# Optimization experiments

Hardware: AMD Instinct MI355X
Metric: run time of the kernel (lower is better)

## Reference

```python
import jax, jax.numpy as jnp
import numpy as np

EPS = 1e-6   # param.eps
DT = 1e-2    # param.dt
DX = 1.0     # param.dx
DY = 1.0     # param.dy
N_PARAM = 1.0  # param.N


def _lap(c, dx=1.0, dy=1.0):
    # 5-point periodic Laplacian stencil on the last two dims
    return ((jnp.roll(c, 1, -1) + jnp.roll(c, -1, -1) - 2.0 * c) / (dx * dx)
            + (jnp.roll(c, 1, -2) + jnp.roll(c, -1, -2) - 2.0 * c) / (dy * dy))


def _log_with_mask(m, eps=EPS):
    # masked positions get constant eps -> zero gradient there, like torch masked_fill
    return jnp.log(jnp.where(m < eps, eps, m))


def setup_inputs() -> dict:
    key = jax.random.key(0)
    ks = jax.random.split(key, 12)
    B, H, W = 8, 1024, 1024
    inp = {
        "cv": jax.random.uniform(ks[0], (B, H, W), dtype=jnp.float32),
        "ci": jax.random.uniform(ks[1], (B, H, W), dtype=jnp.float32),
        "eta": jax.random.uniform(ks[2], (B, H, W), dtype=jnp.float32),
    }
    names = ["energy_v0", "energy_i0", "kBT0", "kappa_v0", "kappa_i0",
             "kappa_eta0", "diff_v0", "diff_i0", "L0"]
    for i, n in enumerate(names):
        inp[n] = jax.random.uniform(ks[3 + i], (1,), dtype=jnp.float32)
    return inp


def reference(cv, ci, eta, energy_v0, energy_i0, kBT0, kappa_v0, kappa_i0,
              kappa_eta0, diff_v0, diff_i0, L0):
    energy_v = jnp.abs(energy_v0) + 0.001
    energy_i = jnp.abs(energy_i0) + 0.001
    kBT = jnp.abs(kBT0) + 0.001
    kappa_v = jnp.abs(kappa_v0) + 0.001
    kappa_i = jnp.abs(kappa_i0) + 0.001
    kappa_eta = jnp.abs(kappa_eta0) + 0.001
    diff_v = jnp.abs(diff_v0) + 0.001
    diff_i = jnp.abs(diff_i0) + 0.001
    L = jnp.abs(L0) + 0.001

    lap_cv = _lap(cv, DX, DY)
    lap_ci = _lap(ci, DX, DY)
    lap_eta = _lap(eta, DX, DY)

    h = (eta - 1.0) ** 2
    j = eta ** 2
    cs = 1.0 - cv - ci
    log_cv = _log_with_mask(cv)
    log_ci = _log_with_mask(ci)
    log_cs = _log_with_mask(cs)

    fs = energy_v * cv + energy_i * ci + kBT * (cv * log_cv + ci * log_ci + cs * log_cs)
    dfs_dcv = energy_v + kBT * (log_cv - log_cs)
    dfs_dci = energy_i + kBT * (log_ci - log_cs)

    fv = (cv - 1.0) ** 2 + ci ** 2
    dfv_dcv = 2.0 * (cv - 1.0)
    dfv_dci = 2.0 * ci

    dF_dcv = h * dfs_dcv + j * dfv_dcv - kappa_v * lap_cv
    dF_dci = h * dfs_dci + j * dfv_dci - kappa_i * lap_ci
    dF_deta = N_PARAM * (fs * 2.0 * (eta - 1.0) + fv * 2.0 * eta - kappa_eta * lap_eta)

    mv = diff_v * cv / kBT
    mi = diff_i * ci / kBT

    cv_new = jnp.clip(cv + DT * (mv * _lap(dF_dcv)), 0.0, 1.0)
    ci_new = jnp.clip(ci + DT * (mi * _lap(dF_dci)), 0.0, 1.0)
    eta_new = jnp.clip(eta + DT * (-L * dF_deta), 0.0, 1.0)
    return cv_new, ci_new, eta_new
```

## Files before the change

kernel.cpp:

```cpp
#include <hip/hip_runtime.h>

#define WMASK 1023
#define LOG2W 10
#define HW (1024 * 1024)

#define EPS 1e-6f
#define DT 1e-2f

#define TX 64
#define TY 16
#define EX (TX + 2)
#define EY (TY + 2)

__device__ __forceinline__ float scal(const float* __restrict__ p) {
    return fabsf(p[0]) + 0.001f;
}
__device__ __forceinline__ float logm(float m) {
    return logf(m < EPS ? EPS : m);
}
__device__ __forceinline__ float clip01(float v) {
    return fminf(fmaxf(v, 0.0f), 1.0f);
}

__global__ __launch_bounds__(256) void irr_fused(
    const float* __restrict__ cv,
    const float* __restrict__ ci,
    const float* __restrict__ eta,
    const float* __restrict__ p_ev,
    const float* __restrict__ p_ei,
    const float* __restrict__ p_kbt,
    const float* __restrict__ p_kv,
    const float* __restrict__ p_ki,
    const float* __restrict__ p_ke,
    const float* __restrict__ p_dv,
    const float* __restrict__ p_di,
    const float* __restrict__ p_L,
    float* __restrict__ cv_new,
    float* __restrict__ ci_new,
    float* __restrict__ eta_new)
{
    __shared__ float sdv[EY][EX];
    __shared__ float sdi[EY][EX];

    const int tid = threadIdx.y * 64 + threadIdx.x;
    const int x0 = blockIdx.x * TX;
    const int y0 = blockIdx.y * TY;
    const int bbase = blockIdx.z * HW;

    const float energy_v = scal(p_ev);
    const float energy_i = scal(p_ei);
    const float kBT      = scal(p_kbt);
    const float kappa_v  = scal(p_kv);
    const float kappa_i  = scal(p_ki);
    const float kappa_e  = scal(p_ke);
    const float diff_v   = scal(p_dv);
    const float diff_i   = scal(p_di);
    const float L        = scal(p_L);

    for (int t = tid; t < EX * EY; t += 256) {
        const int ex = t % EX;
        const int ey = t / EX;
        const int gx = (x0 + ex - 1) & WMASK;
        const int gy = (y0 + ey - 1) & WMASK;
        const int row  = bbase + (gy << LOG2W);
        const int rowm = bbase + (((gy + WMASK) & WMASK) << LOG2W);
        const int rowp = bbase + (((gy + 1) & WMASK) << LOG2W);
        const int xm = (gx + WMASK) & WMASK;
        const int xp = (gx + 1) & WMASK;

        const float c0 = cv[row + gx];
        const float lap_cv = cv[row + xm] + cv[row + xp]
                           + cv[rowm + gx] + cv[rowp + gx] - 4.0f * c0;
        const float i0 = ci[row + gx];
        const float lap_ci = ci[row + xm] + ci[row + xp]
                           + ci[rowm + gx] + ci[rowp + gx] - 4.0f * i0;
        const float e0 = eta[row + gx];
        const float lap_eta = eta[row + xm] + eta[row + xp]
                            + eta[rowm + gx] + eta[rowp + gx] - 4.0f * e0;

        const float h  = (e0 - 1.0f) * (e0 - 1.0f);
        const float jj = e0 * e0;
        const float cs = 1.0f - c0 - i0;
        const float lcv = logm(c0);
        const float lci = logm(i0);
        const float lcs = logm(cs);

        const float fs = energy_v * c0 + energy_i * i0
                       + kBT * (c0 * lcv + i0 * lci + cs * lcs);
        const float dfs_dcv = energy_v + kBT * (lcv - lcs);
        const float dfs_dci = energy_i + kBT * (lci - lcs);

        const float fv = (c0 - 1.0f) * (c0 - 1.0f) + i0 * i0;
        const float dfv_dcv = 2.0f * (c0 - 1.0f);
        const float dfv_dci = 2.0f * i0;

        sdv[ey][ex] = h * dfs_dcv + jj * dfv_dcv - kappa_v * lap_cv;
        sdi[ey][ex] = h * dfs_dci + jj * dfv_dci - kappa_i * lap_ci;

        if (ex >= 1 && ex <= TX && ey >= 1 && ey <= TY) {
            const float dF_deta = fs * 2.0f * (e0 - 1.0f) + fv * 2.0f * e0
                                - kappa_e * lap_eta;
            eta_new[row + gx] = clip01(e0 + DT * (-L * dF_deta));
        }
    }

    __syncthreads();

    const int tx = threadIdx.x;
    for (int ty = threadIdx.y; ty < TY; ty += 4) {
        const int ex = tx + 1;
        const int ey = ty + 1;

        const float v0 = sdv[ey][ex];
        const float lap_v = sdv[ey][ex - 1] + sdv[ey][ex + 1]
                          + sdv[ey - 1][ex] + sdv[ey + 1][ex] - 4.0f * v0;
        const float w0 = sdi[ey][ex];
        const float lap_i = sdi[ey][ex - 1] + sdi[ey][ex + 1]
                          + sdi[ey - 1][ex] + sdi[ey + 1][ex] - 4.0f * w0;

        const int gidx = bbase + ((y0 + ty) << LOG2W) + (x0 + tx);
        const float c0 = cv[gidx];
        const float i0 = ci[gidx];

        const float mv = diff_v * c0 / kBT;
        const float mi = diff_i * i0 / kBT;

        cv_new[gidx] = clip01(c0 + DT * (mv * lap_v));
        ci_new[gidx] = clip01(i0 + DT * (mi * lap_i));
    }
}

extern "C" void kernel_launch(void* const* d_in, const int* in_sizes, int n_in,
                              void* d_out, int out_size, void* d_ws, size_t ws_size,
                              hipStream_t stream) {
    const float* cv  = (const float*)d_in[0];
    const float* ci  = (const float*)d_in[1];
    const float* eta = (const float*)d_in[2];
    const float* p_ev  = (const float*)d_in[3];
    const float* p_ei  = (const float*)d_in[4];
    const float* p_kbt = (const float*)d_in[5];
    const float* p_kv  = (const float*)d_in[6];
    const float* p_ki  = (const float*)d_in[7];
    const float* p_ke  = (const float*)d_in[8];
    const float* p_dv  = (const float*)d_in[9];
    const float* p_di  = (const float*)d_in[10];
    const float* p_L   = (const float*)d_in[11];

    const int N = in_sizes[0];

    float* out     = (float*)d_out;
    float* cv_new  = out;
    float* ci_new  = out + N;
    float* eta_new = out + 2 * N;

    const dim3 block(64, 4, 1);
    const dim3 grid(1024 / TX, 1024 / TY, N / HW);

    irr_fused<<<grid, block, 0, stream>>>(cv, ci, eta, p_ev, p_ei, p_kbt,
                                          p_kv, p_ki, p_ke, p_dv, p_di, p_L,
                                          cv_new, ci_new, eta_new);
}
```

Baseline: 232.3 us.

## Stage input tiles in shared memory with float4 loads and nontemporal stores

Each block now loads a 20x72 halo tile of cv, ci and eta into shared memory with vectorized float4 loads, then computes both stencil passes from LDS instead of issuing redundant scattered global reads. Also switches to fast __logf, precomputes diff/kBT, and writes outputs with nontemporal stores. The trade-offs are much larger shared memory use per block, which may lower occupancy, and slightly less accurate logarithms.

Result: faster. 208.3 us (-10.3%).

```diff
diff --git a/kernel.cpp b/kernel.cpp
--- a/kernel.cpp
+++ b/kernel.cpp
@@ -9,14 +9,16 @@
 
 #define TX 64
 #define TY 16
-#define EX (TX + 2)
-#define EY (TY + 2)
+#define RX 72
+#define RY 20
+#define DXT 66
+#define DYT 18
 
 __device__ __forceinline__ float scal(const float* __restrict__ p) {
     return fabsf(p[0]) + 0.001f;
 }
 __device__ __forceinline__ float logm(float m) {
-    return logf(m < EPS ? EPS : m);
+    return __logf(m < EPS ? EPS : m);
 }
 __device__ __forceinline__ float clip01(float v) {
     return fminf(fmaxf(v, 0.0f), 1.0f);
@@ -39,10 +41,13 @@
     float* __restrict__ ci_new,
     float* __restrict__ eta_new)
 {
-    __shared__ float sdv[EY][EX];
-    __shared__ float sdi[EY][EX];
+    __shared__ float scv[RY][RX];
+    __shared__ float sci[RY][RX];
+    __shared__ float seta[RY][RX];
+    __shared__ float sdv[DYT][DXT];
+    __shared__ float sdi[DYT][DXT];
 
-    const int tid = threadIdx.y * 64 + threadIdx.x;
+    const int tid = threadIdx.x;
     const int x0 = blockIdx.x * TX;
     const int y0 = blockIdx.y * TY;
     const int bbase = blockIdx.z * HW;
@@ -56,27 +61,42 @@
     const float diff_v   = scal(p_dv);
     const float diff_i   = scal(p_di);
     const float L        = scal(p_L);
+    const float rv = diff_v / kBT;
+    const float ri = diff_i / kBT;
 
-    for (int t = tid; t < EX * EY; t += 256) {
-        const int ex = t % EX;
-        const int ey = t / EX;
-        const int gx = (x0 + ex - 1) & WMASK;
-        const int gy = (y0 + ey - 1) & WMASK;
-        const int row  = bbase + (gy << LOG2W);
-        const int rowm = bbase + (((gy + WMASK) & WMASK) << LOG2W);
-        const int rowp = bbase + (((gy + 1) & WMASK) << LOG2W);
-        const int xm = (gx + WMASK) & WMASK;
-        const int xp = (gx + 1) & WMASK;
+    for (int t = tid; t < 3 * 384; t += 256) {
+        const int f = t / 384;
+        const int r = t - f * 384;
+        if (r < 360) {
+            const int cx = r % 18;
+            const int cy = r / 18;
+            const int gx = (x0 - 4 + cx * 4) & WMASK;
+            const int gy = (y0 - 2 + cy) & WMASK;
+            const float* __restrict__ src = (f == 0) ? cv : (f == 1) ? ci : eta;
+            const float4 v = *(const float4*)(src + bbase + (gy << LOG2W) + gx);
+            float* dst = (f == 0) ? &scv[cy][cx * 4]
+                       : (f == 1) ? &sci[cy][cx * 4]
+                                  : &seta[cy][cx * 4];
+            *(float4*)dst = v;
+        }
+    }
+    __syncthreads();
 
-        const float c0 = cv[row + gx];
-        const float lap_cv = cv[row + xm] + cv[row + xp]
-                           + cv[rowm + gx] + cv[rowp + gx] - 4.0f * c0;
-        const float i0 = ci[row + gx];
-        const float lap_ci = ci[row + xm] + ci[row + xp]
-                           + ci[rowm + gx] + ci[rowp + gx] - 4.0f * i0;
-        const float e0 = eta[row + gx];
-        const float lap_eta = eta[row + xm] + eta[row + xp]
-                            + eta[rowm + gx] + eta[rowp + gx] - 4.0f * e0;
+    for (int t = tid; t < DXT * DYT; t += 256) {
+        const int ex = t % DXT;
+        const int ey = t / DXT;
+        const int rx = ex + 3;
+        const int ry = ey + 1;
+
+        const float c0 = scv[ry][rx];
+        const float lap_cv = scv[ry][rx - 1] + scv[ry][rx + 1]
+                           + scv[ry - 1][rx] + scv[ry + 1][rx] - 4.0f * c0;
+        const float i0 = sci[ry][rx];
+        const float lap_ci = sci[ry][rx - 1] + sci[ry][rx + 1]
+                           + sci[ry - 1][rx] + sci[ry + 1][rx] - 4.0f * i0;
+        const float e0 = seta[ry][rx];
+        const float lap_eta = seta[ry][rx - 1] + seta[ry][rx + 1]
+                            + seta[ry - 1][rx] + seta[ry + 1][rx] - 4.0f * e0;
 
         const float h  = (e0 - 1.0f) * (e0 - 1.0f);
         const float jj = e0 * e0;
@@ -91,25 +111,25 @@
         const float dfs_dci = energy_i + kBT * (lci - lcs);
 
         const float fv = (c0 - 1.0f) * (c0 - 1.0f) + i0 * i0;
-        const float dfv_dcv = 2.0f * (c0 - 1.0f);
-        const float dfv_dci = 2.0f * i0;
 
-        sdv[ey][ex] = h * dfs_dcv + jj * dfv_dcv - kappa_v * lap_cv;
-        sdi[ey][ex] = h * dfs_dci + jj * dfv_dci - kappa_i * lap_ci;
+        sdv[ey][ex] = h * dfs_dcv + jj * (2.0f * (c0 - 1.0f)) - kappa_v * lap_cv;
+        sdi[ey][ex] = h * dfs_dci + jj * (2.0f * i0)          - kappa_i * lap_ci;
 
         if (ex >= 1 && ex <= TX && ey >= 1 && ey <= TY) {
             const float dF_deta = fs * 2.0f * (e0 - 1.0f) + fv * 2.0f * e0
                                 - kappa_e * lap_eta;
-            eta_new[row + gx] = clip01(e0 + DT * (-L * dF_deta));
+            const int gidx = bbase + ((y0 + ey - 1) << LOG2W) + (x0 + ex - 1);
+            __builtin_nontemporal_store(clip01(e0 + DT * (-L * dF_deta)),
+                                        &eta_new[gidx]);
         }
     }
-
     __syncthreads();
 
-    const int tx = threadIdx.x;
-    for (int ty = threadIdx.y; ty < TY; ty += 4) {
-        const int ex = tx + 1;
-        const int ey = ty + 1;
+    for (int t = tid; t < TX * TY; t += 256) {
+        const int ox = t & (TX - 1);
+        const int oy = t >> 6;
+        const int ex = ox + 1;
+        const int ey = oy + 1;
 
         const float v0 = sdv[ey][ex];
         const float lap_v = sdv[ey][ex - 1] + sdv[ey][ex + 1]
@@ -118,15 +138,12 @@
         const float lap_i = sdi[ey][ex - 1] + sdi[ey][ex + 1]
                           + sdi[ey - 1][ex] + sdi[ey + 1][ex] - 4.0f * w0;
 
-        const int gidx = bbase + ((y0 + ty) << LOG2W) + (x0 + tx);
-        const float c0 = cv[gidx];
-        const float i0 = ci[gidx];
+        const float c0 = scv[oy + 2][ox + 4];
+        const float i0 = sci[oy + 2][ox + 4];
 
-        const float mv = diff_v * c0 / kBT;
-        const float mi = diff_i * i0 / kBT;
-
-        cv_new[gidx] = clip01(c0 + DT * (mv * lap_v));
-        ci_new[gidx] = clip01(i0 + DT * (mi * lap_i));
+        const int gidx = bbase + ((y0 + oy) << LOG2W) + (x0 + ox);
+        __builtin_nontemporal_store(clip01(c0 + DT * ((rv * c0) * lap_v)), &cv_new[gidx]);
+        __builtin_nontemporal_store(clip01(i0 + DT * ((ri * i0) * lap_i)), &ci_new[gidx]);
     }
 }
 
@@ -153,7 +170,7 @@
     float* ci_new  = out + N;
     float* eta_new = out + 2 * N;
 
-    const dim3 block(64, 4, 1);
+    const dim3 block(256);
     const dim3 grid(1024 / TX, 1024 / TY, N / HW);
 
     irr_fused<<<grid, block, 0, stream>>>(cv, ci, eta, p_ev, p_ei, p_kbt,
```
